# Kernel optimization log

Hardware: AMD Instinct MI355X
Metric: run time of the kernel (lower is better)

The kernel has to match this reference:

```python
import jax, jax.numpy as jnp
import numpy as np
import math

C, N, D, D_CTX = 256, 512, 256, 256
K = 24
HOMEOSTASIS = 0.01
FEEDBACK = 0.3
B = 64


def setup_inputs() -> dict:
    key = jax.random.key(0)
    k1, k2, k3, k4, k5 = jax.random.split(key, 5)
    ff_scale = math.sqrt(2.0 / (D + N))
    ctx_scale = math.sqrt(2.0 / (D_CTX + N))
    pred_scale = math.sqrt(2.0 / (N + D))
    return {
        "x_input": jax.random.normal(k1, (B, D), dtype=jnp.float32),
        "x_context": jax.random.normal(k2, (B, D_CTX), dtype=jnp.float32),
        "W_ff": jax.random.normal(k3, (C, D, N), dtype=jnp.float32) * ff_scale,
        "W_ctx": jax.random.normal(k4, (C, D_CTX, N), dtype=jnp.float32) * ctx_scale,
        "W_pred": jax.random.normal(k5, (C, N, D), dtype=jnp.float32) * pred_scale,
        "bias": jnp.zeros((C, N), dtype=jnp.float32),
        "avg_activity": jnp.full((C, N), 0.05, dtype=jnp.float32),
    }


def _k_winners(drive, avg_activity, k):
    # homeostatic boosting: boost * homeostasis * 100
    boost = jnp.log1p(0.05 / (avg_activity + 1e-6))  # [C, N]
    boosted = drive + boost[None] * (HOMEOSTASIS * 100.0)
    topk_vals = jax.lax.top_k(boosted, k)[0]  # [B, C, k]
    threshold = jax.lax.stop_gradient(topk_vals[..., -1:])  # [B, C, 1]
    mask = (boosted >= threshold).astype(drive.dtype)
    activation = jax.nn.relu(drive) * mask
    activation = activation / (jnp.sum(activation, axis=-1, keepdims=True) + 1e-8) * k
    return activation


def reference(x_input, x_context, W_ff, W_ctx, W_pred, bias, avg_activity):
    # per-column feedforward + context drive: [B, C, N]
    ff_drive = jnp.einsum('bd,cdn->bcn', x_input, W_ff)
    ctx_drive = jnp.einsum('bd,cdn->bcn', x_context, W_ctx)
    drive = ff_drive + ctx_drive * FEEDBACK + bias[None]
    activations = _k_winners(drive, avg_activity, K)  # [B, C, N]
    predictions = jnp.einsum('bcn,cnd->bcd', activations, W_pred)  # [B, C, D]
    errors = x_input[:, None, :] - predictions  # [B, C, D]
    return activations, predictions, errors
```

## Files before the change

kernel.cpp:

```cpp
#include <hip/hip_runtime.h>
#include <math.h>

#define CC 256
#define NN 512
#define DD 256
#define BB 64
#define KK 24
#define WCAP 48

#define XSMEM_BYTES (2 * DD * BB * 4)

__global__ void transpose_x_kernel(const float* __restrict__ x_in,
                                   const float* __restrict__ x_ctx,
                                   float* __restrict__ xT) {
  int idx = blockIdx.x * blockDim.x + threadIdx.x;
  int d = idx >> 6;
  int b = idx & 63;
  float v = (d < DD) ? x_in[b * DD + d] : 0.3f * x_ctx[b * DD + (d - DD)];
  xT[idx] = v;
}

#define FMA16(W, XPTR)                                                        \
  do {                                                                        \
    const float4* __restrict__ xp = reinterpret_cast<const float4*>(XPTR);    \
    const float4 x0 = xp[0], x1 = xp[1], x2 = xp[2], x3 = xp[3];              \
    acc[0].x = fmaf(x0.x, (W).x, acc[0].x);   acc[0].y = fmaf(x0.x, (W).y, acc[0].y);   \
    acc[1].x = fmaf(x0.y, (W).x, acc[1].x);   acc[1].y = fmaf(x0.y, (W).y, acc[1].y);   \
    acc[2].x = fmaf(x0.z, (W).x, acc[2].x);   acc[2].y = fmaf(x0.z, (W).y, acc[2].y);   \
    acc[3].x = fmaf(x0.w, (W).x, acc[3].x);   acc[3].y = fmaf(x0.w, (W).y, acc[3].y);   \
    acc[4].x = fmaf(x1.x, (W).x, acc[4].x);   acc[4].y = fmaf(x1.x, (W).y, acc[4].y);   \
    acc[5].x = fmaf(x1.y, (W).x, acc[5].x);   acc[5].y = fmaf(x1.y, (W).y, acc[5].y);   \
    acc[6].x = fmaf(x1.z, (W).x, acc[6].x);   acc[6].y = fmaf(x1.z, (W).y, acc[6].y);   \
    acc[7].x = fmaf(x1.w, (W).x, acc[7].x);   acc[7].y = fmaf(x1.w, (W).y, acc[7].y);   \
    acc[8].x = fmaf(x2.x, (W).x, acc[8].x);   acc[8].y = fmaf(x2.x, (W).y, acc[8].y);   \
    acc[9].x = fmaf(x2.y, (W).x, acc[9].x);   acc[9].y = fmaf(x2.y, (W).y, acc[9].y);   \
    acc[10].x = fmaf(x2.z, (W).x, acc[10].x); acc[10].y = fmaf(x2.z, (W).y, acc[10].y); \
    acc[11].x = fmaf(x2.w, (W).x, acc[11].x); acc[11].y = fmaf(x2.w, (W).y, acc[11].y); \
    acc[12].x = fmaf(x3.x, (W).x, acc[12].x); acc[12].y = fmaf(x3.x, (W).y, acc[12].y); \
    acc[13].x = fmaf(x3.y, (W).x, acc[13].x); acc[13].y = fmaf(x3.y, (W).y, acc[13].y); \
    acc[14].x = fmaf(x3.z, (W).x, acc[14].x); acc[14].y = fmaf(x3.z, (W).y, acc[14].y); \
    acc[15].x = fmaf(x3.w, (W).x, acc[15].x); acc[15].y = fmaf(x3.w, (W).y, acc[15].y); \
  } while (0)

__launch_bounds__(1024)
__global__ void drive_gemm(const float* __restrict__ xT,
                           const float* __restrict__ W_ff,
                           const float* __restrict__ W_ctx,
                           const float* __restrict__ bias,
                           const float* __restrict__ avg_act,
                           float* __restrict__ driveB) {
  extern __shared__ float xs[];

  const int c = blockIdx.x;
  const int t = threadIdx.x;

  {
    const float4* __restrict__ src = reinterpret_cast<const float4*>(xT);
    float4* dst = reinterpret_cast<float4*>(xs);
#pragma unroll
    for (int i = 0; i < 8; ++i) dst[t + 1024 * i] = src[t + 1024 * i];
  }
  __syncthreads();

  const int n0 = (t & 255) * 2;
  const int b0 = __builtin_amdgcn_readfirstlane((t >> 8) * 16);

  float2 acc[16];
#pragma unroll
  for (int i = 0; i < 16; ++i) { acc[i].x = 0.f; acc[i].y = 0.f; }

#pragma unroll 1
  for (int m = 0; m < 2; ++m) {
    const float* __restrict__ wp =
        (m == 0 ? W_ff : W_ctx) + (size_t)c * DD * NN + n0;
    const float* __restrict__ xb = xs + m * (DD * BB) + b0;

    float2 wa[8], wb[8];
#pragma unroll
    for (int j = 0; j < 8; ++j)
      wa[j] = *reinterpret_cast<const float2*>(wp + (size_t)j * NN);

#pragma unroll 1
    for (int d0 = 0; d0 < DD; d0 += 16) {
#pragma unroll
      for (int j = 0; j < 8; ++j) {
        const int dn = (d0 + 8 + j) & 255;
        wb[j] = *reinterpret_cast<const float2*>(wp + (size_t)dn * NN);
      }
#pragma unroll
      for (int j = 0; j < 8; ++j) FMA16(wa[j], xb + (d0 + j) * BB);
#pragma unroll
      for (int j = 0; j < 8; ++j) {
        const int dn = (d0 + 16 + j) & 255;
        wa[j] = *reinterpret_cast<const float2*>(wp + (size_t)dn * NN);
      }
#pragma unroll
      for (int j = 0; j < 8; ++j) FMA16(wb[j], xb + (d0 + 8 + j) * BB);
    }
  }

  const float2 bz = *reinterpret_cast<const float2*>(bias + (size_t)c * NN + n0);
  const float2 av = *reinterpret_cast<const float2*>(avg_act + (size_t)c * NN + n0);
  float2 bo;
  bo.x = log1pf(0.05f / (av.x + 1e-6f));
  bo.y = log1pf(0.05f / (av.y + 1e-6f));

#pragma unroll
  for (int i = 0; i < 16; ++i) {
    float2 m2;
    m2.x = (acc[i].x + bz.x) + bo.x;
    m2.y = (acc[i].y + bz.y) + bo.y;
    *reinterpret_cast<float2*>(driveB + ((size_t)c * BB + (b0 + i)) * NN + n0) = m2;
  }
}

__launch_bounds__(512)
__global__ void sparse_pred(const float* __restrict__ x_in,
                            const float* __restrict__ driveB,
                            const float* __restrict__ W_pred,
                            const float* __restrict__ avg_act,
                            float* __restrict__ out_act,
                            float* __restrict__ out_pred,
                            float* __restrict__ out_err) {
  __shared__ int wcnt[32];
  __shared__ float wlist[32 * WCAP * 2];

  const int c = blockIdx.x >> 1;
  const int bh = blockIdx.x & 1;
  const int t = threadIdx.x;
  const int lane = t & 63;
  const int wv = t >> 6;

  float bo[8];
#pragma unroll
  for (int j = 0; j < 8; ++j)
    bo[j] = log1pf(0.05f / (avg_act[(size_t)c * NN + lane + 64 * j] + 1e-6f));

  for (int r = wv * 4; r < wv * 4 + 4; ++r) {
    const int b = bh * 32 + r;
    const float* __restrict__ row = driveB + ((size_t)c * BB + b) * NN;
    float o[8], v[8];
#pragma unroll
    for (int j = 0; j < 8; ++j) { o[j] = row[lane + 64 * j]; v[j] = o[j]; }

    float kth = 0.f;
    for (int it = 0; it < KK; ++it) {
      float m = v[0];
#pragma unroll
      for (int j = 1; j < 8; ++j) m = fmaxf(m, v[j]);
#pragma unroll
      for (int off = 1; off <= 32; off <<= 1) m = fmaxf(m, __shfl_xor(m, off));
      kth = m;
      bool mine = false;
#pragma unroll
      for (int j = 0; j < 8; ++j) mine = mine || (v[j] == m);
      unsigned long long msk = __ballot(mine);
      int first = __ffsll(msk) - 1;
      if (lane == first) {
        bool done = false;
#pragma unroll
        for (int j = 0; j < 8; ++j) {
          bool cnd = (!done) && (v[j] == m);
          if (cnd) v[j] = -INFINITY;
          done = done || cnd;
        }
      }
    }

    float raw[8];
    float s = 0.f;
#pragma unroll
    for (int j = 0; j < 8; ++j) {
      const float rw = (o[j] >= kth) ? fmaxf(o[j] - bo[j], 0.f) : 0.f;
      raw[j] = rw;
      s += rw;
    }
#pragma unroll
    for (int off = 1; off <= 32; off <<= 1) s += __shfl_xor(s, off);
    const float sc = (float)KK / (s + 1e-8f);

    int base = 0;
#pragma unroll
    for (int j = 0; j < 8; ++j) {
      const int n = lane + 64 * j;
      const float a = raw[j] * sc;
      out_act[(size_t)b * (CC * NN) + (size_t)c * NN + n] = a;
      const bool win = a > 0.f;
      unsigned long long m = __ballot(win);
      int pos = base + __popcll(m & ((1ull << lane) - 1ull));
      if (win && pos < WCAP) {
        const int slot = (r * WCAP + pos) * 2;
        wlist[slot] = a;
        reinterpret_cast<int*>(wlist)[slot + 1] = n;
      }
      base += (int)__popcll(m);
    }
    if (lane == 0) wcnt[r] = (base < WCAP) ? base : WCAP;
  }
  __syncthreads();

  {
    const int dq = t & 63;
    const int d0 = dq * 4;
    const int grp = t >> 6;
    const float* __restrict__ wp = W_pred + (size_t)c * NN * DD;
    for (int bi = 0; bi < 4; ++bi) {
      const int r = grp * 4 + bi;
      const int b = bh * 32 + r;
      const int cnt = wcnt[r];
      float4 p0 = make_float4(0.f, 0.f, 0.f, 0.f);
      float4 p1 = make_float4(0.f, 0.f, 0.f, 0.f);
      float4 p2 = make_float4(0.f, 0.f, 0.f, 0.f);
      float4 p3 = make_float4(0.f, 0.f, 0.f, 0.f);
      int i = 0;
      for (; i + 4 <= cnt; i += 4) {
        const int s0 = (r * WCAP + i) * 2;
        const float a0 = wlist[s0 + 0];
        const int n0 = reinterpret_cast<const int*>(wlist)[s0 + 1];
        const float a1 = wlist[s0 + 2];
        const int n1 = reinterpret_cast<const int*>(wlist)[s0 + 3];
        const float a2 = wlist[s0 + 4];
        const int n2 = reinterpret_cast<const int*>(wlist)[s0 + 5];
        const float a3 = wlist[s0 + 6];
        const int n3 = reinterpret_cast<const int*>(wlist)[s0 + 7];
        const float4 w0 = *reinterpret_cast<const float4*>(wp + (size_t)n0 * DD + d0);
        const float4 w1 = *reinterpret_cast<const float4*>(wp + (size_t)n1 * DD + d0);
        const float4 w2 = *reinterpret_cast<const float4*>(wp + (size_t)n2 * DD + d0);
        const float4 w3 = *reinterpret_cast<const float4*>(wp + (size_t)n3 * DD + d0);
        p0.x = fmaf(a0, w0.x, p0.x); p0.y = fmaf(a0, w0.y, p0.y);
        p0.z = fmaf(a0, w0.z, p0.z); p0.w = fmaf(a0, w0.w, p0.w);
        p1.x = fmaf(a1, w1.x, p1.x); p1.y = fmaf(a1, w1.y, p1.y);
        p1.z = fmaf(a1, w1.z, p1.z); p1.w = fmaf(a1, w1.w, p1.w);
        p2.x = fmaf(a2, w2.x, p2.x); p2.y = fmaf(a2, w2.y, p2.y);
        p2.z = fmaf(a2, w2.z, p2.z); p2.w = fmaf(a2, w2.w, p2.w);
        p3.x = fmaf(a3, w3.x, p3.x); p3.y = fmaf(a3, w3.y, p3.y);
        p3.z = fmaf(a3, w3.z, p3.z); p3.w = fmaf(a3, w3.w, p3.w);
      }
      for (; i < cnt; ++i) {
        const int s0 = (r * WCAP + i) * 2;
        const float a0 = wlist[s0];
        const int n0 = reinterpret_cast<const int*>(wlist)[s0 + 1];
        const float4 w0 = *reinterpret_cast<const float4*>(wp + (size_t)n0 * DD + d0);
        p0.x = fmaf(a0, w0.x, p0.x); p0.y = fmaf(a0, w0.y, p0.y);
        p0.z = fmaf(a0, w0.z, p0.z); p0.w = fmaf(a0, w0.w, p0.w);
      }
      float4 r4;
      r4.x = (p0.x + p1.x) + (p2.x + p3.x);
      r4.y = (p0.y + p1.y) + (p2.y + p3.y);
      r4.z = (p0.z + p1.z) + (p2.z + p3.z);
      r4.w = (p0.w + p1.w) + (p2.w + p3.w);
      const float4 xi = *reinterpret_cast<const float4*>(x_in + (size_t)b * DD + d0);
      float4 e4;
      e4.x = xi.x - r4.x; e4.y = xi.y - r4.y; e4.z = xi.z - r4.z; e4.w = xi.w - r4.w;
      *reinterpret_cast<float4*>(out_pred + (size_t)b * (CC * DD) + (size_t)c * DD + d0) = r4;
      *reinterpret_cast<float4*>(out_err + (size_t)b * (CC * DD) + (size_t)c * DD + d0) = e4;
    }
  }
}

#define MAT_F (BB * NN)
#define FSMEM_FLOATS (MAT_F + BB + BB + NN + BB + BB * WCAP * 2)
#define FSMEM_BYTES (FSMEM_FLOATS * 4)

__launch_bounds__(1024)
__global__ void cortical_fused(const float* __restrict__ x_in,
                               const float* __restrict__ xT,
                               const float* __restrict__ W_ff,
                               const float* __restrict__ W_ctx,
                               const float* __restrict__ W_pred,
                               const float* __restrict__ bias,
                               const float* __restrict__ avg_act,
                               float* __restrict__ out_act,
                               float* __restrict__ out_pred,
                               float* __restrict__ out_err) {
  extern __shared__ float smem[];
  float* mat = smem;
  float* thr = smem + MAT_F;
  float* scl = thr + BB;
  float* boostS = scl + BB;
  int* wcnt = (int*)(boostS + NN);
  float* wlist = (float*)(wcnt + BB);

  const int c = blockIdx.x;
  const int t = threadIdx.x;
  const int lane = t & 63;
  const int wv = t >> 6;

  if (t < NN) boostS[t] = log1pf(0.05f / (avg_act[c * NN + t] + 1e-6f));
  __syncthreads();

  const int ng = t & 255;
  const int n0 = ng * 2;
  const int b0 = __builtin_amdgcn_readfirstlane((t >> 8) * 16);

  float acc[16][2];
#pragma unroll
  for (int i = 0; i < 16; ++i) { acc[i][0] = 0.f; acc[i][1] = 0.f; }

  const float* __restrict__ wf = W_ff + (size_t)c * DD * NN + n0;
  const float* __restrict__ wc = W_ctx + (size_t)c * DD * NN + n0;

#pragma unroll 4
  for (int d = 0; d < DD; ++d) {
    const float2 w = *reinterpret_cast<const float2*>(wf + (size_t)d * NN);
    const float* __restrict__ xp = xT + d * BB + b0;
#pragma unroll
    for (int i = 0; i < 16; ++i) {
      const float xv = xp[i];
      acc[i][0] = fmaf(xv, w.x, acc[i][0]);
      acc[i][1] = fmaf(xv, w.y, acc[i][1]);
    }
  }
#pragma unroll 4
  for (int d = 0; d < DD; ++d) {
    const float2 w = *reinterpret_cast<const float2*>(wc + (size_t)d * NN);
    const float* __restrict__ xp = xT + (DD + d) * BB + b0;
#pragma unroll
    for (int i = 0; i < 16; ++i) {
      const float xv = xp[i];
      acc[i][0] = fmaf(xv, w.x, acc[i][0]);
      acc[i][1] = fmaf(xv, w.y, acc[i][1]);
    }
  }

  const float2 bz = *reinterpret_cast<const float2*>(bias + (size_t)c * NN + n0);
  const float2 bo = *reinterpret_cast<const float2*>(boostS + n0);
#pragma unroll
  for (int i = 0; i < 16; ++i) {
    float2 m2;
    m2.x = (acc[i][0] + bz.x) + bo.x;
    m2.y = (acc[i][1] + bz.y) + bo.y;
    *reinterpret_cast<float2*>(mat + (size_t)(b0 + i) * NN + n0) = m2;
  }
  __syncthreads();

  for (int r = wv * 4; r < wv * 4 + 4; ++r) {
    float v[8];
#pragma unroll
    for (int j = 0; j < 8; ++j) v[j] = mat[r * NN + lane + 64 * j];
    float kth = 0.f;
    for (int it = 0; it < KK; ++it) {
      float m = v[0];
#pragma unroll
      for (int j = 1; j < 8; ++j) m = fmaxf(m, v[j]);
#pragma unroll
      for (int off = 1; off <= 32; off <<= 1) m = fmaxf(m, __shfl_xor(m, off));
      kth = m;
      bool mine = false;
#pragma unroll
      for (int j = 0; j < 8; ++j) mine = mine || (v[j] == m);
      unsigned long long msk = __ballot(mine);
      int first = __ffsll(msk) - 1;
      if (lane == first) {
        bool done = false;
#pragma unroll
        for (int j = 0; j < 8; ++j) {
          bool cnd = (!done) && (v[j] == m);
          if (cnd) v[j] = -INFINITY;
          done = done || cnd;
        }
      }
    }
    if (lane == 0) thr[r] = kth;
  }
  __syncthreads();

  for (int r = wv * 4; r < wv * 4 + 4; ++r) {
    const float tb = thr[r];
    float raw[8];
    float s = 0.f;
#pragma unroll
    for (int j = 0; j < 8; ++j) {
      const int n = lane + 64 * j;
      const float bv = mat[r * NN + n];
      const float rw = (bv >= tb) ? fmaxf(bv - boostS[n], 0.f) : 0.f;
      raw[j] = rw;
      s += rw;
    }
#pragma unroll
    for (int off = 1; off <= 32; off <<= 1) s += __shfl_xor(s, off);
    const float sc = (float)KK / (s + 1e-8f);

    int base = 0;
#pragma unroll
    for (int j = 0; j < 8; ++j) {
      const int n = lane + 64 * j;
      const float a = raw[j] * sc;
      out_act[(size_t)r * (CC * NN) + (size_t)c * NN + n] = a;
      const bool win = a > 0.f;
      unsigned long long m = __ballot(win);
      int pos = base + __popcll(m & ((1ull << lane) - 1ull));
      if (win && pos < WCAP) {
        const int slot = (r * WCAP + pos) * 2;
        wlist[slot] = a;
        reinterpret_cast<int*>(wlist)[slot + 1] = n;
      }
      base += (int)__popcll(m);
    }
    if (lane == 0) wcnt[r] = (base < WCAP) ? base : WCAP;
  }
  __syncthreads();

  {
    const int dq = t & 63;
    const int d0 = dq * 4;
    const int grp = t >> 6;
    const float* __restrict__ wp = W_pred + (size_t)c * NN * DD;
    for (int bi = 0; bi < 4; ++bi) {
      const int b = grp * 4 + bi;
      const int cnt = wcnt[b];
      float4 p = make_float4(0.f, 0.f, 0.f, 0.f);
      float4 q = make_float4(0.f, 0.f, 0.f, 0.f);
      int i = 0;
      for (; i + 2 <= cnt; i += 2) {
        const int s0 = (b * WCAP + i) * 2;
        const int s1 = s0 + 2;
        const float a0 = wlist[s0];
        const int nn0 = reinterpret_cast<const int*>(wlist)[s0 + 1];
        const float a1 = wlist[s1];
        const int nn1 = reinterpret_cast<const int*>(wlist)[s1 + 1];
        const float4 w0 = *reinterpret_cast<const float4*>(wp + (size_t)nn0 * DD + d0);
        const float4 w1 = *reinterpret_cast<const float4*>(wp + (size_t)nn1 * DD + d0);
        p.x = fmaf(a0, w0.x, p.x); p.y = fmaf(a0, w0.y, p.y);
        p.z = fmaf(a0, w0.z, p.z); p.w = fmaf(a0, w0.w, p.w);
        q.x = fmaf(a1, w1.x, q.x); q.y = fmaf(a1, w1.y, q.y);
        q.z = fmaf(a1, w1.z, q.z); q.w = fmaf(a1, w1.w, q.w);
      }
      if (i < cnt) {
        const int s0 = (b * WCAP + i) * 2;
        const float a0 = wlist[s0];
        const int nn0 = reinterpret_cast<const int*>(wlist)[s0 + 1];
        const float4 w0 = *reinterpret_cast<const float4*>(wp + (size_t)nn0 * DD + d0);
        p.x = fmaf(a0, w0.x, p.x); p.y = fmaf(a0, w0.y, p.y);
        p.z = fmaf(a0, w0.z, p.z); p.w = fmaf(a0, w0.w, p.w);
      }
      float4 r4;
      r4.x = p.x + q.x; r4.y = p.y + q.y; r4.z = p.z + q.z; r4.w = p.w + q.w;
      const float4 xi = *reinterpret_cast<const float4*>(x_in + (size_t)b * DD + d0);
      float4 e4;
      e4.x = xi.x - r4.x; e4.y = xi.y - r4.y; e4.z = xi.z - r4.z; e4.w = xi.w - r4.w;
      *reinterpret_cast<float4*>(out_pred + (size_t)b * (CC * DD) + (size_t)c * DD + d0) = r4;
      *reinterpret_cast<float4*>(out_err + (size_t)b * (CC * DD) + (size_t)c * DD + d0) = e4;
    }
  }
}

extern "C" void kernel_launch(void* const* d_in, const int* in_sizes, int n_in,
                              void* d_out, int out_size, void* d_ws, size_t ws_size,
                              hipStream_t stream) {
  const float* x_in = (const float*)d_in[0];
  const float* x_ctx = (const float*)d_in[1];
  const float* W_ff = (const float*)d_in[2];
  const float* W_ctx = (const float*)d_in[3];
  const float* W_pred = (const float*)d_in[4];
  const float* bias = (const float*)d_in[5];
  const float* avg = (const float*)d_in[6];

  float* out = (float*)d_out;
  float* out_act = out;
  float* out_pred = out + (size_t)BB * CC * NN;
  float* out_err = out_pred + (size_t)BB * CC * DD;

  float* xT = (float*)d_ws;
  float* driveB = xT + 2 * BB * DD;

  const size_t need_bytes = (size_t)(2 * BB * DD + (size_t)CC * BB * NN) * 4;

  transpose_x_kernel<<<(2 * BB * DD) / 256, 256, 0, stream>>>(x_in, x_ctx, xT);

  if (ws_size >= need_bytes) {
    hipFuncSetAttribute((const void*)drive_gemm,
                        hipFuncAttributeMaxDynamicSharedMemorySize, XSMEM_BYTES);
    drive_gemm<<<CC, 1024, XSMEM_BYTES, stream>>>(xT, W_ff, W_ctx, bias, avg,
                                                  driveB);
    sparse_pred<<<2 * CC, 512, 0, stream>>>(x_in, driveB, W_pred, avg, out_act,
                                            out_pred, out_err);
  } else {
    hipFuncSetAttribute((const void*)cortical_fused,
                        hipFuncAttributeMaxDynamicSharedMemorySize, FSMEM_BYTES);
    cortical_fused<<<CC, 1024, FSMEM_BYTES, stream>>>(x_in, xT, W_ff, W_ctx,
                                                      W_pred, bias, avg, out_act,
                                                      out_pred, out_err);
  }
}
```

Baseline: 259.1 us.

## Split reduction dimension across half-blocks and reduce partials through shared memory

The drive GEMM now splits the d dimension between two halves of the 1024-thread block. Each thread holds 32 batch rows by 2 columns of accumulators, twice as many as before, which improves the ratio of weight loads to FMAs. The partial sums from the second half are passed through shared memory and added by the first half before the bias/boost epilogue. The explicit double-buffered weight prefetch is dropped in favour of an unroll-4 loop, and launch_bounds gains a min-blocks hint. The larger accumulator set raises register pressure and may cause spills, and the explicit load/compute overlap is lost.

```diff
diff --git a/kernel.cpp b/kernel.cpp
--- a/kernel.cpp
+++ b/kernel.cpp
@@ -20,29 +20,7 @@
   xT[idx] = v;
 }
 
-#define FMA16(W, XPTR)                                                        \
-  do {                                                                        \
-    const float4* __restrict__ xp = reinterpret_cast<const float4*>(XPTR);    \
-    const float4 x0 = xp[0], x1 = xp[1], x2 = xp[2], x3 = xp[3];              \
-    acc[0].x = fmaf(x0.x, (W).x, acc[0].x);   acc[0].y = fmaf(x0.x, (W).y, acc[0].y);   \
-    acc[1].x = fmaf(x0.y, (W).x, acc[1].x);   acc[1].y = fmaf(x0.y, (W).y, acc[1].y);   \
-    acc[2].x = fmaf(x0.z, (W).x, acc[2].x);   acc[2].y = fmaf(x0.z, (W).y, acc[2].y);   \
-    acc[3].x = fmaf(x0.w, (W).x, acc[3].x);   acc[3].y = fmaf(x0.w, (W).y, acc[3].y);   \
-    acc[4].x = fmaf(x1.x, (W).x, acc[4].x);   acc[4].y = fmaf(x1.x, (W).y, acc[4].y);   \
-    acc[5].x = fmaf(x1.y, (W).x, acc[5].x);   acc[5].y = fmaf(x1.y, (W).y, acc[5].y);   \
-    acc[6].x = fmaf(x1.z, (W).x, acc[6].x);   acc[6].y = fmaf(x1.z, (W).y, acc[6].y);   \
-    acc[7].x = fmaf(x1.w, (W).x, acc[7].x);   acc[7].y = fmaf(x1.w, (W).y, acc[7].y);   \
-    acc[8].x = fmaf(x2.x, (W).x, acc[8].x);   acc[8].y = fmaf(x2.x, (W).y, acc[8].y);   \
-    acc[9].x = fmaf(x2.y, (W).x, acc[9].x);   acc[9].y = fmaf(x2.y, (W).y, acc[9].y);   \
-    acc[10].x = fmaf(x2.z, (W).x, acc[10].x); acc[10].y = fmaf(x2.z, (W).y, acc[10].y); \
-    acc[11].x = fmaf(x2.w, (W).x, acc[11].x); acc[11].y = fmaf(x2.w, (W).y, acc[11].y); \
-    acc[12].x = fmaf(x3.x, (W).x, acc[12].x); acc[12].y = fmaf(x3.x, (W).y, acc[12].y); \
-    acc[13].x = fmaf(x3.y, (W).x, acc[13].x); acc[13].y = fmaf(x3.y, (W).y, acc[13].y); \
-    acc[14].x = fmaf(x3.z, (W).x, acc[14].x); acc[14].y = fmaf(x3.z, (W).y, acc[14].y); \
-    acc[15].x = fmaf(x3.w, (W).x, acc[15].x); acc[15].y = fmaf(x3.w, (W).y, acc[15].y); \
-  } while (0)
-
-__launch_bounds__(1024)
+__launch_bounds__(1024, 4)
 __global__ void drive_gemm(const float* __restrict__ xT,
                            const float* __restrict__ W_ff,
                            const float* __restrict__ W_ctx,
@@ -62,12 +40,15 @@
   }
   __syncthreads();
 
-  const int n0 = (t & 255) * 2;
-  const int b0 = __builtin_amdgcn_readfirstlane((t >> 8) * 16);
-
-  float2 acc[16];
-#pragma unroll
-  for (int i = 0; i < 16; ++i) { acc[i].x = 0.f; acc[i].y = 0.f; }
+  const int dh = __builtin_amdgcn_readfirstlane(t >> 9);
+  const int tt = t & 511;
+  const int n0 = (tt & 255) * 2;
+  const int b0 = __builtin_amdgcn_readfirstlane((tt >> 8) * 32);
+  const int dlo = dh * 128;
+
+  float2 acc[32];
+#pragma unroll
+  for (int i = 0; i < 32; ++i) { acc[i].x = 0.f; acc[i].y = 0.f; }
 
 #pragma unroll 1
   for (int m = 0; m < 2; ++m) {
@@ -75,42 +56,48 @@
         (m == 0 ? W_ff : W_ctx) + (size_t)c * DD * NN + n0;
     const float* __restrict__ xb = xs + m * (DD * BB) + b0;
 
-    float2 wa[8], wb[8];
-#pragma unroll
-    for (int j = 0; j < 8; ++j)
-      wa[j] = *reinterpret_cast<const float2*>(wp + (size_t)j * NN);
-
-#pragma unroll 1
-    for (int d0 = 0; d0 < DD; d0 += 16) {
-#pragma unroll
-      for (int j = 0; j < 8; ++j) {
-        const int dn = (d0 + 8 + j) & 255;
-        wb[j] = *reinterpret_cast<const float2*>(wp + (size_t)dn * NN);
-      }
-#pragma unroll
-      for (int j = 0; j < 8; ++j) FMA16(wa[j], xb + (d0 + j) * BB);
-#pragma unroll
-      for (int j = 0; j < 8; ++j) {
-        const int dn = (d0 + 16 + j) & 255;
-        wa[j] = *reinterpret_cast<const float2*>(wp + (size_t)dn * NN);
-      }
-#pragma unroll
-      for (int j = 0; j < 8; ++j) FMA16(wb[j], xb + (d0 + 8 + j) * BB);
-    }
-  }
-
-  const float2 bz = *reinterpret_cast<const float2*>(bias + (size_t)c * NN + n0);
-  const float2 av = *reinterpret_cast<const float2*>(avg_act + (size_t)c * NN + n0);
-  float2 bo;
-  bo.x = log1pf(0.05f / (av.x + 1e-6f));
-  bo.y = log1pf(0.05f / (av.y + 1e-6f));
-
-#pragma unroll
-  for (int i = 0; i < 16; ++i) {
-    float2 m2;
-    m2.x = (acc[i].x + bz.x) + bo.x;
-    m2.y = (acc[i].y + bz.y) + bo.y;
-    *reinterpret_cast<float2*>(driveB + ((size_t)c * BB + (b0 + i)) * NN + n0) = m2;
+#pragma unroll 4
+    for (int d = dlo; d < dlo + 128; ++d) {
+      const float2 w = *reinterpret_cast<const float2*>(wp + (size_t)d * NN);
+      const float4* __restrict__ xp =
+          reinterpret_cast<const float4*>(xb + (size_t)d * BB);
+#pragma unroll
+      for (int q = 0; q < 8; ++q) {
+        const float4 xv = xp[q];
+        acc[q * 4 + 0].x = fmaf(xv.x, w.x, acc[q * 4 + 0].x);
+        acc[q * 4 + 0].y = fmaf(xv.x, w.y, acc[q * 4 + 0].y);
+        acc[q * 4 + 1].x = fmaf(xv.y, w.x, acc[q * 4 + 1].x);
+        acc[q * 4 + 1].y = fmaf(xv.y, w.y, acc[q * 4 + 1].y);
+        acc[q * 4 + 2].x = fmaf(xv.z, w.x, acc[q * 4 + 2].x);
+        acc[q * 4 + 2].y = fmaf(xv.z, w.y, acc[q * 4 + 2].y);
+        acc[q * 4 + 3].x = fmaf(xv.w, w.x, acc[q * 4 + 3].x);
+        acc[q * 4 + 3].y = fmaf(xv.w, w.y, acc[q * 4 + 3].y);
+      }
+    }
+  }
+
+  __syncthreads();
+  if (dh == 1) {
+#pragma unroll
+    for (int i = 0; i < 32; ++i) {
+      xs[(2 * i) * 512 + tt] = acc[i].x;
+      xs[(2 * i + 1) * 512 + tt] = acc[i].y;
+    }
+  }
+  __syncthreads();
+  if (dh == 0) {
+    const float2 bz = *reinterpret_cast<const float2*>(bias + (size_t)c * NN + n0);
+    const float2 av = *reinterpret_cast<const float2*>(avg_act + (size_t)c * NN + n0);
+    float2 bo;
+    bo.x = log1pf(0.05f / (av.x + 1e-6f));
+    bo.y = log1pf(0.05f / (av.y + 1e-6f));
+#pragma unroll
+    for (int i = 0; i < 32; ++i) {
+      float2 m2;
+      m2.x = (acc[i].x + xs[(2 * i) * 512 + tt]) + bz.x + bo.x;
+      m2.y = (acc[i].y + xs[(2 * i + 1) * 512 + tt]) + bz.y + bo.y;
+      *reinterpret_cast<float2*>(driveB + ((size_t)c * BB + (b0 + i)) * NN + n0) = m2;
+    }
   }
 }
 
```

New measurement: 427.2 us. 64.9% more time.
